# Kernel tuning notes

Hardware: AMD Instinct MI355X
Metric: run time of the kernel (lower is better)

Reference implementation:

```python
import jax, jax.numpy as jnp
import numpy as np
import math

DIM = 1024
NUM_HEADS = 16
HEAD_DIM = DIM // NUM_HEADS
EPS = 1e-6
DILATED = 2
WINDOW = 2  # window_size init arg; actual window = L * WINDOW per side


def setup_inputs() -> dict:
    key = jax.random.key(0)
    ks = jax.random.split(key, 14)
    B, S = 1, 8704
    x = jax.random.normal(ks[0], (B, S, DIM), jnp.float32)
    ang = jax.random.uniform(ks[1], (S, HEAD_DIM // 2), jnp.float32, -jnp.pi, jnp.pi)
    freqs_cos = jnp.cos(ang)
    freqs_sin = jnp.sin(ang)
    def lin(k):
        return 0.02 * jax.random.normal(k, (DIM, DIM), jnp.float32)
    def bias(k):
        return 0.01 * jax.random.normal(k, (DIM,), jnp.float32)
    return {
        'x': x, 'freqs_cos': freqs_cos, 'freqs_sin': freqs_sin,
        'wq': lin(ks[2]), 'bq': bias(ks[3]),
        'wk': lin(ks[4]), 'bk': bias(ks[5]),
        'wv': lin(ks[6]), 'bv': bias(ks[7]),
        'wo': lin(ks[8]), 'bo': bias(ks[9]),
        'gq': 1.0 + 0.02 * jax.random.normal(ks[10], (DIM,), jnp.float32),
        'gk': 1.0 + 0.02 * jax.random.normal(ks[11], (DIM,), jnp.float32),
        'f': 34, 'L': 256,
    }


def rmsnorm(h, g):
    return h * jax.lax.rsqrt(jnp.mean(h * h, axis=-1, keepdims=True) + EPS) * g


def rope(h, cos, sin):
    # h: [B,S,D] viewed as interleaved complex pairs per head, rotated by unit freqs
    B, S, D = h.shape
    hp = h.reshape(B, S, NUM_HEADS, HEAD_DIM // 2, 2)
    a, b = hp[..., 0], hp[..., 1]
    c = cos[None, :, None, :]
    s = sin[None, :, None, :]
    ra = a * c - b * s
    rb = a * s + b * c
    return jnp.stack([ra, rb], axis=-1).reshape(B, S, D)


def windowed_attention(q, k, v, w):
    # sliding-window attention: query i attends keys j with |i-j| <= w (inclusive)
    B, S, D = q.shape
    H, hd = NUM_HEADS, HEAD_DIM
    def heads(t):
        return t.reshape(B, S, H, hd).transpose(0, 2, 1, 3)  # [B,H,S,hd]
    qh, kh, vh = heads(q), heads(k), heads(v)
    C = w  # block size == window -> only 3 neighbor key blocks per query block
    pad = (-S) % C
    Sp = S + pad
    nb = Sp // C
    def blocks(t):
        return jnp.pad(t, ((0, 0), (0, 0), (0, pad), (0, 0))).reshape(B, H, nb, C, hd)
    qb = blocks(qh)
    def win(t):
        tb = jnp.pad(blocks(t), ((0, 0), (0, 0), (1, 1), (0, 0), (0, 0)))
        return jnp.concatenate([tb[:, :, i:i + nb] for i in range(3)], axis=3)  # [B,H,nb,3C,hd]
    kw_, vw_ = win(kh), win(vh)
    scores = jnp.einsum('bhnqd,bhnkd->bhnqk', qb, kw_) * (1.0 / math.sqrt(hd))
    qi = jnp.arange(nb)[:, None, None] * C + jnp.arange(C)[None, :, None]      # [nb,C,1]
    kj = (jnp.arange(nb)[:, None, None] - 1) * C + jnp.arange(3 * C)[None, None, :]  # [nb,1,3C]
    valid = (kj >= 0) & (kj < S) & (qi - kj <= w) & (kj - qi <= w)
    scores = jnp.where(valid, scores, -1e9)
    p = jax.nn.softmax(scores, axis=-1)
    o = jnp.einsum('bhnqk,bhnkd->bhnqd', p, vw_)
    return o.reshape(B, H, Sp, hd)[:, :, :S].transpose(0, 2, 1, 3).reshape(B, S, D)


def reference(x, freqs_cos, freqs_sin, wq, bq, wk, bk, wv, bv, wo, bo, gq, gk, f, L):
    B, S, D = x.shape
    q = rope(rmsnorm(x @ wq + bq, gq), freqs_cos, freqs_sin)
    k = rope(rmsnorm(x @ wk + bk, gk), freqs_cos, freqs_sin)
    v = x @ wv + bv
    w = L * WINDOW
    use_dilated = DILATED > 1 and S // (DILATED * L) > 1
    if use_dilated:
        blk = DILATED * L
        pad_len = blk - S % blk  # == blk when S % blk == 0 (faithful to torch code)
        Sp = S + pad_len
        n = Sp // blk
        def padd(t):
            return jnp.pad(t, ((0, 0), (0, pad_len), (0, 0)))
        def dil(t):
            # 'b (n d l) c -> (b d) (n l) c'
            return t.reshape(B, n, DILATED, L, D).transpose(0, 2, 1, 3, 4).reshape(B * DILATED, n * L, D)
        q, k, v = dil(padd(q)), dil(padd(k)), dil(padd(v))
    o = windowed_attention(q, k, v, w)
    out = o @ wo + bo
    if use_dilated:
        # '(b d) (n l) c -> b (n d l) c', then drop pad
        out = out.reshape(B, DILATED, n, L, D).transpose(0, 2, 1, 3, 4).reshape(B, n * DILATED * L, D)
        out = out[:, :S]
    return out
```

## Files before the change

kernel.cpp:

```cpp
#include <hip/hip_runtime.h>
#include <hip/hip_bf16.h>
#include <stdint.h>

#define DIM 1024
#define NH 16
#define HD 64
#define S_ORIG 8704
#define WIN 512

typedef __attribute__((ext_vector_type(8))) short short8;
typedef __attribute__((ext_vector_type(4))) float f32x4;

__device__ __forceinline__ float bf2f(unsigned short u) {
    return __uint_as_float(((unsigned int)u) << 16);
}
__device__ __forceinline__ unsigned short f2bf(float f) {
    unsigned int x = __float_as_uint(f);
    unsigned int r = x + 0x7fffu + ((x >> 16) & 1u);
    return (unsigned short)(r >> 16);
}
__device__ __forceinline__ unsigned int cvtpk(float lo, float hi) {
    unsigned int r;
    asm("v_cvt_pk_bf16_f32 %0, %1, %2" : "=v"(r) : "v"(lo), "v"(hi));
    return r;
}
__device__ __forceinline__ float fexp2(float x) {
#if __has_builtin(__builtin_amdgcn_exp2f)
    return __builtin_amdgcn_exp2f(x);
#else
    float r;
    asm("v_exp_f32 %0, %1" : "=v"(r) : "v"(x));
    return r;
#endif
}

#define GLD_LDS(gptr, lptr) \
    __builtin_amdgcn_global_load_lds((const __attribute__((address_space(1))) void*)(gptr), \
                                     (__attribute__((address_space(3))) void*)(lptr), 16, 0, 0)

__global__ __launch_bounds__(256) void prep(const float* __restrict__ x,
                                            unsigned short* __restrict__ xb,
                                            const float* __restrict__ w0,
                                            const float* __restrict__ w1,
                                            const float* __restrict__ w2,
                                            const float* __restrict__ w3,
                                            unsigned short* __restrict__ wt) {
    __shared__ float ts[64][65];
    const int bx = blockIdx.x;
    const int t = threadIdx.x;
    if (bx < 8704) {
        int i = (bx * 256 + t) * 4;
        float4 v = *(const float4*)(x + i);
        ushort4 o;
        o.x = f2bf(v.x); o.y = f2bf(v.y); o.z = f2bf(v.z); o.w = f2bf(v.w);
        *(ushort4*)(xb + i) = o;
        return;
    }
    const int b = bx - 8704;
    const int z = b >> 8;
    const int rem = b & 255;
    const int kb = (rem >> 4) * 64, nb = (rem & 15) * 64;
    const float* w = z == 0 ? w0 : z == 1 ? w1 : z == 2 ? w2 : w3;
    unsigned short* o = wt + (size_t)z * DIM * DIM;
    const int c = t & 63, r4 = t >> 6;
#pragma unroll
    for (int rr = 0; rr < 16; rr++) {
        int row = rr * 4 + r4;
        ts[row][c] = w[(size_t)(kb + row) * DIM + nb + c];
    }
    __syncthreads();
#pragma unroll
    for (int rr = 0; rr < 16; rr++) {
        int nl = rr * 4 + r4;
        o[(size_t)(nb + nl) * DIM + kb + c] = f2bf(ts[c][nl]);
    }
}

template <int OUTF32>
__global__ __launch_bounds__(256) void gemm_bf16(const unsigned short* __restrict__ A,
                                                 const unsigned short* __restrict__ Bt,
                                                 const float* __restrict__ b0,
                                                 const float* __restrict__ b1,
                                                 const float* __restrict__ b2,
                                                 void* __restrict__ Cout) {
    __shared__ __align__(16) unsigned short As[128 * 32];
    __shared__ __align__(16) unsigned short Bs[128 * 32];
    const int z = blockIdx.z;
    const unsigned short* B = Bt + (size_t)z * DIM * DIM;
    const float* bias = z == 0 ? b0 : (z == 1 ? b1 : b2);
    const int m0 = blockIdx.x * 128, n0 = blockIdx.y * 128;
    const int tid = threadIdx.x;
    const int lane = tid & 63, wv = tid >> 6;
    const int wr = wv >> 1, wc = wv & 1;
    const int quad = lane >> 4, r = lane & 15;

    f32x4 acc[4][4];
#pragma unroll
    for (int i = 0; i < 4; i++)
#pragma unroll
        for (int j = 0; j < 4; j++)
#pragma unroll
            for (int t4 = 0; t4 < 4; t4++) acc[i][j][t4] = 0.0f;

    const unsigned short* a_base = A + (size_t)m0 * DIM;
    const unsigned short* b_base = B + (size_t)n0 * DIM;
    const int c0 = wv * 128 + lane;
    const int r0 = c0 >> 2, o0 = (((c0 & 3) ^ ((c0 >> 3) & 3))) * 8;
    const int c1 = c0 + 64;
    const int r1 = c1 >> 2, o1 = (((c1 & 3) ^ ((c1 >> 3) & 3))) * 8;
    unsigned short* lA0 = &As[(size_t)(wv * 128) * 8];
    unsigned short* lA1 = &As[(size_t)(wv * 128 + 64) * 8];
    unsigned short* lB0 = &Bs[(size_t)(wv * 128) * 8];
    unsigned short* lB1 = &Bs[(size_t)(wv * 128 + 64) * 8];

    const int jsw = (quad ^ ((r >> 1) & 3)) * 8;

    for (int k0 = 0; k0 < DIM; k0 += 32) {
        __syncthreads();
        GLD_LDS(a_base + (size_t)r0 * DIM + k0 + o0, lA0);
        GLD_LDS(a_base + (size_t)r1 * DIM + k0 + o1, lA1);
        GLD_LDS(b_base + (size_t)r0 * DIM + k0 + o0, lB0);
        GLD_LDS(b_base + (size_t)r1 * DIM + k0 + o1, lB1);
        __syncthreads();
        short8 af[4], bfr[4];
#pragma unroll
        for (int i = 0; i < 4; i++)
            af[i] = *(const short8*)&As[(wr * 64 + i * 16 + r) * 32 + jsw];
#pragma unroll
        for (int j = 0; j < 4; j++)
            bfr[j] = *(const short8*)&Bs[(wc * 64 + j * 16 + r) * 32 + jsw];
#pragma unroll
        for (int i = 0; i < 4; i++)
#pragma unroll
            for (int j = 0; j < 4; j++)
                acc[i][j] = __builtin_amdgcn_mfma_f32_16x16x32_bf16(af[i], bfr[j], acc[i][j], 0, 0, 0);
    }

#pragma unroll
    for (int i = 0; i < 4; i++) {
        const int row = m0 + wr * 64 + i * 16 + quad * 4;
#pragma unroll
        for (int j = 0; j < 4; j++) {
            const int col = n0 + wc * 64 + j * 16 + r;
            const float bvl = bias[col];
#pragma unroll
            for (int t4 = 0; t4 < 4; t4++) {
                float vv = acc[i][j][t4] + bvl;
                if (OUTF32) {
                    ((float*)Cout)[(size_t)(row + t4) * DIM + col] = vv;
                } else {
                    ((unsigned short*)Cout)[(size_t)z * S_ORIG * DIM + (size_t)(row + t4) * DIM + col] = f2bf(vv);
                }
            }
        }
    }
}

__global__ __launch_bounds__(256) void norm_rope(unsigned short* __restrict__ hq,
                                                 unsigned short* __restrict__ hk,
                                                 const float* __restrict__ gq,
                                                 const float* __restrict__ gk,
                                                 const float* __restrict__ fcos,
                                                 const float* __restrict__ fsin) {
    const int z = blockIdx.y;
    unsigned short* h = z == 0 ? hq : hk;
    const float* g = z == 0 ? gq : gk;
    const int w = threadIdx.x >> 6, lane = threadIdx.x & 63;
    const int srow = blockIdx.x * 4 + w;
    unsigned short* hp = h + (size_t)srow * DIM;
    const int p0 = lane * 8, p1 = 512 + lane * 8;

    union { int4 i4; unsigned short u[8]; } r0, r1, o0, o1;
    r0.i4 = *(const int4*)(hp + p0);
    r1.i4 = *(const int4*)(hp + p1);
    float v[16];
#pragma unroll
    for (int j = 0; j < 8; j++) { v[j] = bf2f(r0.u[j]); v[8 + j] = bf2f(r1.u[j]); }

    float ss = 0.0f;
#pragma unroll
    for (int j = 0; j < 16; j++) ss += v[j] * v[j];
#pragma unroll
    for (int off = 1; off < 64; off <<= 1) ss += __shfl_xor(ss, off, 64);
    const float rinv = rsqrtf(ss * (1.0f / DIM) + 1e-6f);

    float4 ga = *(const float4*)(g + p0), gb = *(const float4*)(g + p0 + 4);
    float4 gc = *(const float4*)(g + p1), gd = *(const float4*)(g + p1 + 4);
    const float* gg[4] = {&ga.x, &gb.x, &gc.x, &gd.x};
#pragma unroll
    for (int q4 = 0; q4 < 4; q4++)
#pragma unroll
        for (int j = 0; j < 4; j++) v[q4 * 4 + j] *= rinv * gg[q4][j];

    const int i0 = (p0 & 63) >> 1;
    float4 cs = *(const float4*)(fcos + (size_t)srow * 32 + i0);
    float4 sn = *(const float4*)(fsin + (size_t)srow * 32 + i0);
    const float* cp = &cs.x;
    const float* sp = &sn.x;
#pragma unroll
    for (int seg = 0; seg < 2; seg++) {
        unsigned short* uo = seg == 0 ? o0.u : o1.u;
#pragma unroll
        for (int pr = 0; pr < 4; pr++) {
            const float a = v[seg * 8 + pr * 2], b = v[seg * 8 + pr * 2 + 1];
            uo[pr * 2]     = f2bf(a * cp[pr] - b * sp[pr]);
            uo[pr * 2 + 1] = f2bf(a * sp[pr] + b * cp[pr]);
        }
    }
    *(int4*)(hp + p0) = o0.i4;
    *(int4*)(hp + p1) = o1.i4;
}

__device__ __forceinline__ void qstep(const unsigned short* __restrict__ Ks,
                                      const unsigned short* __restrict__ Vt,
                                      unsigned short* __restrict__ pw,
                                      int jsw0, int jsw1, int quad, int r16,
                                      int kbase, int qi, bool edge,
                                      const short8* __restrict__ qf,
                                      f32x4* __restrict__ oacc, float& lsum) {
    f32x4 sv[4];
#pragma unroll
    for (int nt = 0; nt < 4; nt++) {
        const int row = (nt * 16 + r16) * 64;
        short8 k0f = *(const short8*)&Ks[row + jsw0];
        short8 k1f = *(const short8*)&Ks[row + jsw1];
        f32x4 a = {0.0f, 0.0f, 0.0f, 0.0f};
        a = __builtin_amdgcn_mfma_f32_16x16x32_bf16(k0f, qf[0], a, 0, 0, 0);
        a = __builtin_amdgcn_mfma_f32_16x16x32_bf16(k1f, qf[1], a, 0, 0, 0);
        sv[nt] = a;
    }
#pragma unroll
    for (int nt = 0; nt < 4; nt++) {
        float p[4];
#pragma unroll
        for (int rr = 0; rr < 4; rr++) {
            float e = fexp2(sv[nt][rr]);
            if (edge) {
                const int kj = kbase + nt * 16 + quad * 4 + rr;
                const int dl = qi - kj;
                if (dl > WIN || dl < -WIN) e = 0.0f;
            }
            p[rr] = e;
        }
        lsum += (p[0] + p[1]) + (p[2] + p[3]);
        uint2 pk;
        pk.x = cvtpk(p[0], p[1]);
        pk.y = cvtpk(p[2], p[3]);
        *(uint2*)&pw[r16 * 72 + nt * 16 + quad * 4] = pk;
    }
    __asm__ volatile("s_waitcnt lgkmcnt(0)" ::: "memory");
    short8 pf0 = *(const short8*)&pw[r16 * 72 + quad * 8];
    short8 pf1 = *(const short8*)&pw[r16 * 72 + 32 + quad * 8];
#pragma unroll
    for (int nt = 0; nt < 4; nt++) {
        short8 v0f = *(const short8*)&Vt[(nt * 16 + r16) * 72 + quad * 8];
        short8 v1f = *(const short8*)&Vt[(nt * 16 + r16) * 72 + 32 + quad * 8];
        oacc[nt] = __builtin_amdgcn_mfma_f32_16x16x32_bf16(v0f, pf0, oacc[nt], 0, 0, 0);
        oacc[nt] = __builtin_amdgcn_mfma_f32_16x16x32_bf16(v1f, pf1, oacc[nt], 0, 0, 0);
    }
}

__global__ __launch_bounds__(256) void attn(const unsigned short* __restrict__ qkv,
                                            unsigned short* __restrict__ ob) {
    __shared__ __align__(16) unsigned short Ks[64 * 64];
    __shared__ __align__(16) unsigned short Vt[64 * 72];
    __shared__ __align__(16) unsigned short Ps[4][16 * 72];

    const int head = blockIdx.x >> 1;
    const int d = blockIdx.x & 1;
    const int t0 = blockIdx.y * 2, t1 = t0 + 1;
    const int tid = threadIdx.x;
    const int lane = tid & 63, wv = tid >> 6;
    const int quad = lane >> 4, r16 = lane & 15;

    const unsigned short* qb = qkv;
    const unsigned short* kb = qkv + (size_t)S_ORIG * DIM;
    const unsigned short* vb = qkv + (size_t)2 * S_ORIG * DIM;

    const int qi0 = t0 * 64 + wv * 16 + r16;
    const int qi1 = qi0 + 64;
    const int og_q0 = ((qi0 >> 8) << 9) + d * 256 + (qi0 & 255);
    const int og_q1 = ((qi1 >> 8) << 9) + d * 256 + (qi1 & 255);
    short8 qf0[2], qf1[2];
    {
        const float QSC = 0.125f * 1.44269504088896f;
        const unsigned short* qr0 = qb + (size_t)og_q0 * DIM + head * HD + quad * 8;
        const unsigned short* qr1 = qb + (size_t)og_q1 * DIM + head * HD + quad * 8;
#pragma unroll
        for (int c = 0; c < 2; c++) {
            union { int4 i4; unsigned short u[8]; short8 s8; } i0v, i1v, a0v, a1v;
            i0v.i4 = *(const int4*)(qr0 + c * 32);
            i1v.i4 = *(const int4*)(qr1 + c * 32);
#pragma unroll
            for (int j = 0; j < 8; j++) {
                a0v.u[j] = f2bf(bf2f(i0v.u[j]) * QSC);
                a1v.u[j] = f2bf(bf2f(i1v.u[j]) * QSC);
            }
            qf0[c] = a0v.s8;
            qf1[c] = a1v.s8;
        }
    }

    f32x4 oacc0[4], oacc1[4];
    float lsum0 = 0.0f, lsum1 = 0.0f;
#pragma unroll
    for (int nt = 0; nt < 4; nt++)
#pragma unroll
        for (int rr = 0; rr < 4; rr++) { oacc0[nt][rr] = 0.0f; oacc1[nt][rr] = 0.0f; }

    const int kt_lo = (t0 - 8 > 0) ? (t0 - 8) : 0;
    const int kt_hi = (t1 + 8 < 67) ? (t1 + 8) : 67;

    const int krow0 = tid >> 3;
    const int kgc = ((tid & 7) ^ (krow0 & 7)) * 8;
    unsigned short* kdst0 = &Ks[(size_t)(wv * 64) * 8];
    unsigned short* kdst1 = &Ks[(size_t)(256 + wv * 64) * 8];

    const int vt_kk = (tid & 31) * 2, vt_d0 = (tid >> 5) * 8;

    const int jsw0 = (quad ^ (r16 & 7)) * 8;
    const int jsw1 = jsw0 ^ 32;

    unsigned short* pw = &Ps[wv][0];

    for (int kt = kt_lo; kt <= kt_hi; kt++) {
        const int kbase = kt * 64;
        __syncthreads();

        {
            const int kj0 = kbase + krow0;
            const int ok0 = ((kj0 >> 8) << 9) + d * 256 + (kj0 & 255);
            GLD_LDS(kb + (size_t)ok0 * DIM + head * HD + kgc, kdst0);
            const int kj1 = kj0 + 32;
            const int ok1 = ((kj1 >> 8) << 9) + d * 256 + (kj1 & 255);
            GLD_LDS(kb + (size_t)ok1 * DIM + head * HD + kgc, kdst1);
        }
        {
            const int kj0 = kbase + vt_kk;
            const int ok0 = ((kj0 >> 8) << 9) + d * 256 + (kj0 & 255);
            union { int4 i4; unsigned int w[4]; } a0, a1;
            a0.i4 = *(const int4*)(vb + (size_t)ok0 * DIM + head * HD + vt_d0);
            a1.i4 = *(const int4*)(vb + (size_t)(ok0 + 1) * DIM + head * HD + vt_d0);
#pragma unroll
            for (int dw = 0; dw < 4; dw++) {
                unsigned int lo = __builtin_amdgcn_perm(a1.w[dw], a0.w[dw], 0x05040100u);
                unsigned int hi = __builtin_amdgcn_perm(a1.w[dw], a0.w[dw], 0x07060302u);
                *(unsigned int*)&Vt[(vt_d0 + dw * 2) * 72 + vt_kk] = lo;
                *(unsigned int*)&Vt[(vt_d0 + dw * 2 + 1) * 72 + vt_kk] = hi;
            }
        }
        __syncthreads();

        if (kt <= t0 + 8)
            qstep(Ks, Vt, pw, jsw0, jsw1, quad, r16, kbase, qi0,
                  (kt == t0 - 8) || (kt == t0 + 8), qf0, oacc0, lsum0);
        if (kt >= t1 - 8)
            qstep(Ks, Vt, pw, jsw0, jsw1, quad, r16, kbase, qi1,
                  (kt == t1 - 8) || (kt == t1 + 8), qf1, oacc1, lsum1);
    }

    lsum0 += __shfl_xor(lsum0, 16, 64);
    lsum0 += __shfl_xor(lsum0, 32, 64);
    lsum1 += __shfl_xor(lsum1, 16, 64);
    lsum1 += __shfl_xor(lsum1, 32, 64);
    {
        const int cnt0 = (qi0 + WIN < 4607 ? qi0 + WIN : 4607) - 4351;
        if (cnt0 > 0) lsum0 += (float)cnt0;
        const int cnt1 = (qi1 + WIN < 4607 ? qi1 + WIN : 4607) - 4351;
        if (cnt1 > 0) lsum1 += (float)cnt1;
    }
    const float linv0 = 1.0f / lsum0;
    const float linv1 = 1.0f / lsum1;

#pragma unroll
    for (int nt = 0; nt < 4; nt++) {
        ushort4 o0, o1;
        o0.x = f2bf(oacc0[nt][0] * linv0);
        o0.y = f2bf(oacc0[nt][1] * linv0);
        o0.z = f2bf(oacc0[nt][2] * linv0);
        o0.w = f2bf(oacc0[nt][3] * linv0);
        *(ushort4*)&ob[(size_t)og_q0 * DIM + head * HD + nt * 16 + quad * 4] = o0;
        o1.x = f2bf(oacc1[nt][0] * linv1);
        o1.y = f2bf(oacc1[nt][1] * linv1);
        o1.z = f2bf(oacc1[nt][2] * linv1);
        o1.w = f2bf(oacc1[nt][3] * linv1);
        *(ushort4*)&ob[(size_t)og_q1 * DIM + head * HD + nt * 16 + quad * 4] = o1;
    }
}

extern "C" void kernel_launch(void* const* d_in, const int* in_sizes, int n_in,
                              void* d_out, int out_size, void* d_ws, size_t ws_size,
                              hipStream_t stream) {
    const float* x    = (const float*)d_in[0];
    const float* fcos = (const float*)d_in[1];
    const float* fsin = (const float*)d_in[2];
    const float* wq   = (const float*)d_in[3];
    const float* bq   = (const float*)d_in[4];
    const float* wk   = (const float*)d_in[5];
    const float* bk   = (const float*)d_in[6];
    const float* wv   = (const float*)d_in[7];
    const float* bv   = (const float*)d_in[8];
    const float* wo   = (const float*)d_in[9];
    const float* bo   = (const float*)d_in[10];
    const float* gq   = (const float*)d_in[11];
    const float* gk   = (const float*)d_in[12];

    char* ws = (char*)d_ws;
    unsigned short* xb = (unsigned short*)(ws);
    unsigned short* wt = (unsigned short*)(ws + 17825792);
    unsigned short* h  = (unsigned short*)(ws + 26214400);
    unsigned short* ob = (unsigned short*)(ws + 79691776);
    float* outp = (float*)d_out;

    prep<<<9728, 256, 0, stream>>>(x, xb, wq, wk, wv, wo, wt);
    gemm_bf16<0><<<dim3(68, 8, 3), 256, 0, stream>>>(xb, wt, bq, bk, bv, (void*)h);
    norm_rope<<<dim3(2176, 2), 256, 0, stream>>>(h, h + (size_t)S_ORIG * DIM, gq, gk, fcos, fsin);
    attn<<<dim3(32, 34), 256, 0, stream>>>(h, ob);
    gemm_bf16<1><<<dim3(68, 8, 1), 256, 0, stream>>>(ob, wt + (size_t)3 * DIM * DIM, bo, bo, bo, (void*)outp);
}
```

Measured before the change: 312.6 us.

## Double-buffer K tiles and prefetch V registers in windowed attention loop

The attention loop now issues the next key tile's global-to-LDS loads into a second K buffer and prefetches the next V rows into registers before computing on the current tile. Manual vmcnt waits and raw barriers replace the two __syncthreads per iteration. The goal is to hide global memory latency behind the MFMA work. The cost is doubled K LDS, extra VGPRs for the prefetched V, and a redundant load on the last iteration.

```diff
diff --git a/kernel.cpp b/kernel.cpp
--- a/kernel.cpp
+++ b/kernel.cpp
@@ -37,6 +37,10 @@
 #define GLD_LDS(gptr, lptr) \
     __builtin_amdgcn_global_load_lds((const __attribute__((address_space(1))) void*)(gptr), \
                                      (__attribute__((address_space(3))) void*)(lptr), 16, 0, 0)
+
+#define FBAR() do { __asm__ volatile("" ::: "memory"); \
+                    __builtin_amdgcn_s_barrier(); \
+                    __asm__ volatile("" ::: "memory"); } while (0)
 
 __global__ __launch_bounds__(256) void prep(const float* __restrict__ x,
                                             unsigned short* __restrict__ xb,
@@ -260,9 +264,22 @@
     }
 }
 
+__device__ __forceinline__ void pack_write_v(unsigned short* __restrict__ Vt,
+                                             int4 a0i, int4 a1i, int vt_d0, int vt_kk) {
+    union { int4 i4; unsigned int w[4]; } a0, a1;
+    a0.i4 = a0i; a1.i4 = a1i;
+#pragma unroll
+    for (int dw = 0; dw < 4; dw++) {
+        unsigned int lo = __builtin_amdgcn_perm(a1.w[dw], a0.w[dw], 0x05040100u);
+        unsigned int hi = __builtin_amdgcn_perm(a1.w[dw], a0.w[dw], 0x07060302u);
+        *(unsigned int*)&Vt[(vt_d0 + dw * 2) * 72 + vt_kk] = lo;
+        *(unsigned int*)&Vt[(vt_d0 + dw * 2 + 1) * 72 + vt_kk] = hi;
+    }
+}
+
 __global__ __launch_bounds__(256) void attn(const unsigned short* __restrict__ qkv,
                                             unsigned short* __restrict__ ob) {
-    __shared__ __align__(16) unsigned short Ks[64 * 64];
+    __shared__ __align__(16) unsigned short Ks[2][64 * 64];
     __shared__ __align__(16) unsigned short Vt[64 * 72];
     __shared__ __align__(16) unsigned short Ps[4][16 * 72];
 
@@ -313,8 +330,6 @@
 
     const int krow0 = tid >> 3;
     const int kgc = ((tid & 7) ^ (krow0 & 7)) * 8;
-    unsigned short* kdst0 = &Ks[(size_t)(wv * 64) * 8];
-    unsigned short* kdst1 = &Ks[(size_t)(256 + wv * 64) * 8];
 
     const int vt_kk = (tid & 31) * 2, vt_d0 = (tid >> 5) * 8;
 
@@ -323,41 +338,59 @@
 
     unsigned short* pw = &Ps[wv][0];
 
+#define ISSUE_K(kbase_, bufb_) do {                                              \
+        const int kj0_ = (kbase_) + krow0;                                       \
+        const int ok0_ = ((kj0_ >> 8) << 9) + d * 256 + (kj0_ & 255);            \
+        GLD_LDS(kb + (size_t)ok0_ * DIM + head * HD + kgc, (bufb_) + wv * 512);  \
+        const int kj1_ = kj0_ + 32;                                              \
+        const int ok1_ = ((kj1_ >> 8) << 9) + d * 256 + (kj1_ & 255);            \
+        GLD_LDS(kb + (size_t)ok1_ * DIM + head * HD + kgc, (bufb_) + 2048 + wv * 512); \
+    } while (0)
+
+#define LOAD_V(kbase_, a0_, a1_) do {                                            \
+        const int kj_ = (kbase_) + vt_kk;                                        \
+        const int ok_ = ((kj_ >> 8) << 9) + d * 256 + (kj_ & 255);               \
+        (a0_) = *(const int4*)(vb + (size_t)ok_ * DIM + head * HD + vt_d0);      \
+        (a1_) = *(const int4*)(vb + (size_t)(ok_ + 1) * DIM + head * HD + vt_d0);\
+    } while (0)
+
+    ISSUE_K(kt_lo * 64, &Ks[0][0]);
+    int4 vc0, vc1;
+    LOAD_V(kt_lo * 64, vc0, vc1);
+
+    int cur = 0;
     for (int kt = kt_lo; kt <= kt_hi; kt++) {
         const int kbase = kt * 64;
-        __syncthreads();
-
-        {
-            const int kj0 = kbase + krow0;
-            const int ok0 = ((kj0 >> 8) << 9) + d * 256 + (kj0 & 255);
-            GLD_LDS(kb + (size_t)ok0 * DIM + head * HD + kgc, kdst0);
-            const int kj1 = kj0 + 32;
-            const int ok1 = ((kj1 >> 8) << 9) + d * 256 + (kj1 & 255);
-            GLD_LDS(kb + (size_t)ok1 * DIM + head * HD + kgc, kdst1);
-        }
-        {
-            const int kj0 = kbase + vt_kk;
-            const int ok0 = ((kj0 >> 8) << 9) + d * 256 + (kj0 & 255);
-            union { int4 i4; unsigned int w[4]; } a0, a1;
-            a0.i4 = *(const int4*)(vb + (size_t)ok0 * DIM + head * HD + vt_d0);
-            a1.i4 = *(const int4*)(vb + (size_t)(ok0 + 1) * DIM + head * HD + vt_d0);
-#pragma unroll
-            for (int dw = 0; dw < 4; dw++) {
-                unsigned int lo = __builtin_amdgcn_perm(a1.w[dw], a0.w[dw], 0x05040100u);
-                unsigned int hi = __builtin_amdgcn_perm(a1.w[dw], a0.w[dw], 0x07060302u);
-                *(unsigned int*)&Vt[(vt_d0 + dw * 2) * 72 + vt_kk] = lo;
-                *(unsigned int*)&Vt[(vt_d0 + dw * 2 + 1) * 72 + vt_kk] = hi;
-            }
-        }
-        __syncthreads();
+        FBAR();
+
+        const int knb = ((kt < kt_hi) ? (kt + 1) : kt_hi) * 64;
+        ISSUE_K(knb, &Ks[cur ^ 1][0]);
+        int4 vn0, vn1;
+        LOAD_V(knb, vn0, vn1);
+
+        __asm__ volatile("s_waitcnt vmcnt(4)" ::: "memory");
+        __builtin_amdgcn_sched_barrier(0);
+
+        pack_write_v(&Vt[0], vc0, vc1, vt_d0, vt_kk);
+        __asm__ volatile("s_waitcnt lgkmcnt(0)" ::: "memory");
+        FBAR();
 
         if (kt <= t0 + 8)
-            qstep(Ks, Vt, pw, jsw0, jsw1, quad, r16, kbase, qi0,
+            qstep(&Ks[cur][0], Vt, pw, jsw0, jsw1, quad, r16, kbase, qi0,
                   (kt == t0 - 8) || (kt == t0 + 8), qf0, oacc0, lsum0);
         if (kt >= t1 - 8)
-            qstep(Ks, Vt, pw, jsw0, jsw1, quad, r16, kbase, qi1,
+            qstep(&Ks[cur][0], Vt, pw, jsw0, jsw1, quad, r16, kbase, qi1,
                   (kt == t1 - 8) || (kt == t1 + 8), qf1, oacc1, lsum1);
-    }
+
+        vc0 = vn0; vc1 = vn1;
+        cur ^= 1;
+    }
+#undef ISSUE_K
+#undef LOAD_V
+
+    __asm__ volatile("" :: "v"(vc0.x), "v"(vc0.y), "v"(vc0.z), "v"(vc0.w),
+                          "v"(vc1.x), "v"(vc1.y), "v"(vc1.z), "v"(vc1.w));
+    __asm__ volatile("s_waitcnt vmcnt(0)" ::: "memory");
 
     lsum0 += __shfl_xor(lsum0, 16, 64);
     lsum0 += __shfl_xor(lsum0, 32, 64);
```

New measurement: 312.2 us. No clear change (-0.1%).
